# Performance work log

Measured on AMD Instinct MI355X. Metric: run time of the kernel, lower is better.

Reference implementation:

```python
import jax, jax.numpy as jnp
import numpy as np

N = 100_000      # nodes
E = 800_000      # edges (avg degree 8)
IN = 64          # in_channels
OUT = 64         # out_channels
HEADS = 4
HD = OUT // HEADS  # per-head out channels (concat=True)


def _unif(key, shape, fan_in):
    b = 1.0 / np.sqrt(fan_in)
    return jax.random.uniform(key, shape, jnp.float32, -b, b)


def setup_inputs() -> dict:
    key = jax.random.key(0)
    ks = jax.random.split(key, 12)
    x = jax.random.normal(ks[0], (N, IN), jnp.float32)
    pos = jax.random.normal(ks[1], (N, 3), jnp.float32)
    edge_index = jax.random.randint(ks[2], (2, E), 0, N, jnp.int32)
    # Per-head PointTransformerConv params (stacked over heads).
    # lin / lin_src / lin_dst are bias-free Linear(in, hd); pos_nn is Linear(3, hd) with bias.
    W_lin = _unif(ks[3], (HEADS, IN, HD), IN)
    W_src = _unif(ks[4], (HEADS, IN, HD), IN)
    W_dst = _unif(ks[5], (HEADS, IN, HD), IN)
    W_pos = _unif(ks[6], (HEADS, 3, HD), 3)
    b_pos = _unif(ks[7], (HEADS, HD), 3)
    # projection MLP: Linear(OUT,OUT) -> ReLU -> Linear(OUT,OUT)
    W1 = _unif(ks[8], (OUT, OUT), OUT)
    b1 = _unif(ks[9], (OUT,), OUT)
    W2 = _unif(ks[10], (OUT, OUT), OUT)
    b2 = _unif(ks[11], (OUT,), OUT)
    return dict(x=x, pos=pos, edge_index=edge_index, W_lin=W_lin, W_src=W_src,
                W_dst=W_dst, W_pos=W_pos, b_pos=b_pos, W1=W1, b1=b1, W2=W2, b2=b2)


def reference(x, pos, edge_index, W_lin, W_src, W_dst, W_pos, b_pos, W1, b1, W2, b2):
    # Add self-loops (PointTransformerConv default add_self_loops=True).
    loops = jnp.arange(N, dtype=edge_index.dtype)
    src = jnp.concatenate([edge_index[0], loops])   # j (source)
    dst = jnp.concatenate([edge_index[1], loops])   # i (target)

    # Per-node, all-heads projections: [N, H, HD]
    v = jnp.einsum('ni,hio->nho', x, W_lin)
    a_src = jnp.einsum('ni,hio->nho', x, W_src)
    a_dst = jnp.einsum('ni,hio->nho', x, W_dst)

    # Relative-position encoding delta = pos_nn(pos_i - pos_j): [Et, H, HD]
    rel = pos[dst] - pos[src]
    delta = jnp.einsum('ec,hco->eho', rel, W_pos) + b_pos

    # Attention logits per edge/channel: alpha_i - alpha_j + delta
    alpha = a_dst[dst] - a_src[src] + delta

    # Segment softmax over incoming edges of each target node (numerically stable).
    amax = jax.ops.segment_max(alpha, dst, num_segments=N)
    amax = jnp.where(jnp.isfinite(amax), amax, 0.0)
    ex = jnp.exp(alpha - amax[dst])
    denom = jax.ops.segment_sum(ex, dst, num_segments=N)
    attn = ex / jnp.maximum(denom[dst], 1e-16)

    # Message = attn * (lin(x_j) + delta), scatter-sum to targets: [N, H, HD]
    msg = attn * (v[src] + delta)
    out_h = jax.ops.segment_sum(msg, dst, num_segments=N)

    # Concat heads -> projection MLP
    out = out_h.reshape(N, HEADS * HD)
    h = jax.nn.relu(out @ W1 + b1)
    return h @ W2 + b2
```

## Files before the change

### kernel.cpp

```cpp
#include <hip/hip_runtime.h>
#include <math.h>


typedef _Float16 f16;
typedef _Float16 f16x2 __attribute__((ext_vector_type(2)));
typedef _Float16 f16x4 __attribute__((ext_vector_type(4)));
typedef _Float16 f16x8 __attribute__((ext_vector_type(8)));
typedef float f32x4 __attribute__((ext_vector_type(4)));

#define A_PITCH 104
#define C_PITCH 200
#define LOG2E 1.44269504f
#define S_CAP 32

__global__ __launch_bounds__(256) void zero_wprep_kernel(
    int Zb, int* __restrict__ cnt, int N,
    const float* __restrict__ Ws, const float* __restrict__ Wl,
    const float* __restrict__ Wp, const float* __restrict__ bp,
    const float* __restrict__ W1, const float* __restrict__ W2,
    f16* __restrict__ Bt, f16* __restrict__ W1p, f16* __restrict__ W2p)
{
    if ((int)blockIdx.x < Zb) {
        int i4 = (blockIdx.x * 256 + threadIdx.x) * 4;
        if (i4 + 3 < N) {
            *(int4*)&cnt[i4] = make_int4(0, 0, 0, 0);
        } else {
            for (int i = i4; i < N; i++) cnt[i] = 0;
        }
        return;
    }
    int idx = (blockIdx.x - Zb) * 256 + threadIdx.x;
    if (idx < 192 * 96) {
        int col = idx / 96, k = idx - col * 96;
        float v = 0.f;
        if (col < 128) {
            int p = col >> 1, h = p >> 4, o = p & 15;
            if (col & 1) {
                if (k < 64)      v = Wl[h * 1024 + k * 16 + o];
                else if (k < 67) v = -Wp[h * 48 + (k - 64) * 16 + o];
            } else {
                if (k < 64)      v = -LOG2E * Ws[h * 1024 + k * 16 + o];
                else if (k < 67) v = -LOG2E * Wp[h * 48 + (k - 64) * 16 + o];
            }
        } else {
            int c = col - 128, h = c >> 4, o = c & 15;
            if (k >= 64 && k < 67) v = Wp[h * 48 + (k - 64) * 16 + o];
            else if (k == 67)      v = bp[c];
        }
        Bt[col * 96 + k] = (f16)v;
    } else if (idx < 192 * 96 + 4096) {
        int t = idx - 192 * 96;
        int col = t >> 6, k = t & 63;
        W1p[col * 64 + k] = (f16)W1[k * 64 + col];
    } else if (idx < 192 * 96 + 8192) {
        int t = idx - 192 * 96 - 4096;
        int col = t >> 6, k = t & 63;
        W2p[col * 64 + k] = (f16)W2[k * 64 + col];
    }
}

__global__ __launch_bounds__(256) void gemm_hist_kernel(
    const float* __restrict__ x, const float* __restrict__ pos,
    const f16* __restrict__ Bt,
    f16* __restrict__ AV, f16* __restrict__ G, int N, int Gb,
    const int* __restrict__ ei, int E, int Hb2,
    int* __restrict__ cnt, int* __restrict__ ssrc)
{
    __shared__ f16 smem[64 * C_PITCH];
    int tid = threadIdx.x;

    if (blockIdx.x & 1) {
        int hb = blockIdx.x >> 1;
        if (hb >= Hb2) return;
        int e0 = hb * 512 + tid;
        int e1 = e0 + 256;
        int s0 = 0, d0 = 0, s1 = 0, d1 = 0;
        bool a0 = e0 < E, a1 = e1 < E;
        if (a0) { s0 = ei[e0]; d0 = ei[E + e0]; }
        if (a1) { s1 = ei[e1]; d1 = ei[E + e1]; }
        if (a0) {
            int r = atomicAdd(&cnt[d0], 1);
            if (r < S_CAP) ssrc[d0 * S_CAP + r] = s0;
        }
        if (a1) {
            int r = atomicAdd(&cnt[d1], 1);
            if (r < S_CAP) ssrc[d1 * S_CAP + r] = s1;
        }
        return;
    }

    int gb = blockIdx.x >> 1;
    if (gb >= Gb) return;
    int l = tid & 63, wv = tid >> 6;
    int quad = l >> 4, lr = l & 15;
    int nb = gb * 64;

    for (int it = 0; it < 4; it++) {
        int q = it * 256 + tid;
        int n = q >> 4, k = (q & 15) * 4;
        float4 xv = make_float4(0.f, 0.f, 0.f, 0.f);
        if (nb + n < N) xv = *(const float4*)&x[(size_t)(nb + n) * 64 + k];
        f16x4 h4; h4[0] = (f16)xv.x; h4[1] = (f16)xv.y; h4[2] = (f16)xv.z; h4[3] = (f16)xv.w;
        *(f16x4*)&smem[n * A_PITCH + k] = h4;
    }
    {
        int n = tid >> 2, seg = tid & 3;
        f16x4 z = {(f16)0, (f16)0, (f16)0, (f16)0};
        f16x4 h4 = z;
        if (seg == 0 && nb + n < N) {
            h4[0] = (f16)pos[(size_t)(nb + n) * 3 + 0];
            h4[1] = (f16)pos[(size_t)(nb + n) * 3 + 1];
            h4[2] = (f16)pos[(size_t)(nb + n) * 3 + 2];
            h4[3] = (f16)1.0f;
        }
        *(f16x4*)&smem[n * A_PITCH + 64 + seg * 8] = h4;
        *(f16x4*)&smem[n * A_PITCH + 64 + seg * 8 + 4] = z;
    }
    __syncthreads();

    f16x8 af[4][3];
    #pragma unroll
    for (int mt = 0; mt < 4; mt++)
        #pragma unroll
        for (int kt = 0; kt < 3; kt++)
            af[mt][kt] = *(const f16x8*)&smem[(mt * 16 + lr) * A_PITCH + kt * 32 + quad * 8];
    __syncthreads();

    #pragma unroll
    for (int t = 0; t < 3; t++) {
        int colBase = (wv * 3 + t) * 16;
        f16x8 b0 = *(const f16x8*)&Bt[(colBase + lr) * 96 + 0  + quad * 8];
        f16x8 b1 = *(const f16x8*)&Bt[(colBase + lr) * 96 + 32 + quad * 8];
        f16x8 b2 = *(const f16x8*)&Bt[(colBase + lr) * 96 + 64 + quad * 8];
        #pragma unroll
        for (int mt = 0; mt < 4; mt++) {
            f32x4 acc = {0.f, 0.f, 0.f, 0.f};
            acc = __builtin_amdgcn_mfma_f32_16x16x32_f16(af[mt][0], b0, acc, 0, 0, 0);
            acc = __builtin_amdgcn_mfma_f32_16x16x32_f16(af[mt][1], b1, acc, 0, 0, 0);
            acc = __builtin_amdgcn_mfma_f32_16x16x32_f16(af[mt][2], b2, acc, 0, 0, 0);
            int col = colBase + lr;
            #pragma unroll
            for (int r = 0; r < 4; r++) {
                int row = mt * 16 + quad * 4 + r;
                smem[row * C_PITCH + col] = (f16)acc[r];
            }
        }
    }
    __syncthreads();

    for (int it = 0; it < 4; it++) {
        int cid = it * 256 + tid;
        int row = cid >> 4, off = (cid & 15) * 8;
        if (nb + row < N)
            *(f16x8*)&AV[(size_t)(nb + row) * 128 + off] =
                *(const f16x8*)&smem[row * C_PITCH + off];
    }
    for (int it = 0; it < 2; it++) {
        int cid = it * 256 + tid;
        int row = cid >> 3, off = (cid & 7) * 8;
        if (nb + row < N)
            *(f16x8*)&G[(size_t)(nb + row) * 64 + off] =
                *(const f16x8*)&smem[row * C_PITCH + 128 + off];
    }
}

__global__ __launch_bounds__(256) void attn_mlp_kernel(
    const f16* __restrict__ AV, const f16* __restrict__ G,
    const int* __restrict__ cnt, const int* __restrict__ ssrc,
    const f16* __restrict__ W1p, const f16* __restrict__ W2p,
    const float* __restrict__ b1, const float* __restrict__ b2,
    float* __restrict__ out, int N)
{
    __shared__ f16 As[32 * 72];
    __shared__ f16 Hs[32 * 72];
    int tid = threadIdx.x, c = tid & 63, wv = tid >> 6;
    int quad = c >> 4, lr = c & 15;
    int nb = blockIdx.x * 32;

    const f16x2* AV2 = (const f16x2*)AV;

    for (int t = 0; t < 8; t++) {
        int i = __builtin_amdgcn_readfirstlane(nb + wv * 8 + t);
        float oh = 0.f;
        if (i < N) {
            float Gi = (float)G[(size_t)i * 64 + c];
            f16x2 wi = AV2[(size_t)i * 64 + c];
            float e0 = __builtin_amdgcn_exp2f((float)wi[0]);
            float num = e0 * (float)wi[1];
            float den = e0;
            int deg = __builtin_amdgcn_readfirstlane(cnt[i]);
            if (deg > S_CAP) deg = S_CAP;
            int base = i * S_CAP;
            for (int k = 0; k < deg; k += 8) {
                int j[8];
                #pragma unroll
                for (int s = 0; s < 8; s++) {
                    int jj = __builtin_amdgcn_readfirstlane(ssrc[base + k + s]);
                    jj = jj < 0 ? 0 : (jj >= N ? N - 1 : jj);
                    j[s] = jj;
                }
                f16x2 w[8];
                #pragma unroll
                for (int s = 0; s < 8; s++) w[s] = AV2[(size_t)j[s] * 64 + c];
                #pragma unroll
                for (int s = 0; s < 8; s++) {
                    float e = __builtin_amdgcn_exp2f((float)w[s][0]);
                    e = (k + s < deg) ? e : 0.f;
                    num = fmaf(e, (float)w[s][1], num);
                    den += e;
                }
            }
            oh = num / den + Gi;
        }
        As[(wv * 8 + t) * 72 + c] = (f16)oh;
    }
    __syncthreads();

    f16x8 af[2][2];
    #pragma unroll
    for (int mt = 0; mt < 2; mt++)
        #pragma unroll
        for (int kt = 0; kt < 2; kt++)
            af[mt][kt] = *(const f16x8*)&As[(mt * 16 + lr) * 72 + kt * 32 + quad * 8];

    int col = wv * 16 + lr;
    f16x8 wb0 = *(const f16x8*)&W1p[col * 64 + quad * 8];
    f16x8 wb1 = *(const f16x8*)&W1p[col * 64 + 32 + quad * 8];
    float bias1 = b1[col];
    #pragma unroll
    for (int mt = 0; mt < 2; mt++) {
        f32x4 acc = {0.f, 0.f, 0.f, 0.f};
        acc = __builtin_amdgcn_mfma_f32_16x16x32_f16(af[mt][0], wb0, acc, 0, 0, 0);
        acc = __builtin_amdgcn_mfma_f32_16x16x32_f16(af[mt][1], wb1, acc, 0, 0, 0);
        #pragma unroll
        for (int r = 0; r < 4; r++) {
            int row = mt * 16 + quad * 4 + r;
            Hs[row * 72 + col] = (f16)fmaxf(acc[r] + bias1, 0.f);
        }
    }
    __syncthreads();

    f16x8 ag[2][2];
    #pragma unroll
    for (int mt = 0; mt < 2; mt++)
        #pragma unroll
        for (int kt = 0; kt < 2; kt++)
            ag[mt][kt] = *(const f16x8*)&Hs[(mt * 16 + lr) * 72 + kt * 32 + quad * 8];

    f16x8 wc0 = *(const f16x8*)&W2p[col * 64 + quad * 8];
    f16x8 wc1 = *(const f16x8*)&W2p[col * 64 + 32 + quad * 8];
    float bias2 = b2[col];
    #pragma unroll
    for (int mt = 0; mt < 2; mt++) {
        f32x4 acc = {0.f, 0.f, 0.f, 0.f};
        acc = __builtin_amdgcn_mfma_f32_16x16x32_f16(ag[mt][0], wc0, acc, 0, 0, 0);
        acc = __builtin_amdgcn_mfma_f32_16x16x32_f16(ag[mt][1], wc1, acc, 0, 0, 0);
        #pragma unroll
        for (int r = 0; r < 4; r++) {
            int row = nb + mt * 16 + quad * 4 + r;
            if (row < N) out[(size_t)row * 64 + col] = acc[r] + bias2;
        }
    }
}

extern "C" void kernel_launch(void* const* d_in, const int* in_sizes, int n_in,
                              void* d_out, int out_size, void* d_ws, size_t ws_size,
                              hipStream_t stream)
{
    const float* x    = (const float*)d_in[0];
    const float* pos  = (const float*)d_in[1];
    const int*   ei   = (const int*)d_in[2];
    const float* Wl   = (const float*)d_in[3];
    const float* Ws   = (const float*)d_in[4];
    const float* Wp   = (const float*)d_in[6];
    const float* bpos = (const float*)d_in[7];
    const float* W1   = (const float*)d_in[8];
    const float* b1   = (const float*)d_in[9];
    const float* W2   = (const float*)d_in[10];
    const float* b2   = (const float*)d_in[11];
    float* out = (float*)d_out;

    const int N = in_sizes[0] / 64;
    const int E = in_sizes[2] / 2;

    char* w = (char*)d_ws;
    f16*  AV   = (f16*)w;                   w += (size_t)N * 128 * 2;
    f16*  G    = (f16*)w;                   w += (size_t)N * 64 * 2;
    f16*  Bt   = (f16*)w;                   w += 192 * 96 * 2;
    f16*  W1p  = (f16*)w;                   w += 4096 * 2;
    f16*  W2p  = (f16*)w;                   w += 4096 * 2;
    int*  cnt  = (int*)w;                   w += (size_t)N * 4;
    int*  ssrc = (int*)w;                   w += (size_t)N * S_CAP * 4;

    const int Zb  = (N + 1023) / 1024;
    const int Pb  = (192 * 96 + 8192 + 255) / 256;
    const int Gb  = (N + 63) / 64;
    const int Hb2 = (E + 511) / 512;
    const int Kb  = (Gb > Hb2 ? Gb : Hb2) * 2;

    zero_wprep_kernel<<<Zb + Pb, 256, 0, stream>>>(Zb, cnt, N, Ws, Wl, Wp, bpos,
                                                   W1, W2, Bt, W1p, W2p);
    gemm_hist_kernel<<<Kb, 256, 0, stream>>>(x, pos, Bt, AV, G, N, Gb,
                                             ei, E, Hb2, cnt, ssrc);
    attn_mlp_kernel<<<(N + 31) / 32, 256, 0, stream>>>(AV, G, cnt, ssrc, W1p, W2p,
                                                       b1, b2, out, N);
}
```

Baseline: 180.2 us.

## Precompute exp weights per source node and gather two targets at once

The projection kernel now applies exp2 to each source node's logit once and stores the pair (e, e*v) in AV, replacing the raw (logit, value) pair. The attention kernel then only sums the gathered pairs instead of running exp per edge. It also processes two target nodes per iteration, interleaving their gathers to keep more memory loads in flight. The cost is that exp values are stored in fp16 with no max subtraction, which risks overflow or precision loss. Out-of-range neighbour indices are also now mapped to 0 rather than clamped.

```diff
diff --git a/kernel.cpp b/kernel.cpp
--- a/kernel.cpp
+++ b/kernel.cpp
@@ -151,9 +151,18 @@
     for (int it = 0; it < 4; it++) {
         int cid = it * 256 + tid;
         int row = cid >> 4, off = (cid & 15) * 8;
-        if (nb + row < N)
-            *(f16x8*)&AV[(size_t)(nb + row) * 128 + off] =
-                *(const f16x8*)&smem[row * C_PITCH + off];
+        if (nb + row < N) {
+            f16x8 w8 = *(const f16x8*)&smem[row * C_PITCH + off];
+            f16x8 o;
+            #pragma unroll
+            for (int p = 0; p < 4; p++) {
+                float e  = __builtin_amdgcn_exp2f((float)w8[2 * p]);
+                float ev = e * (float)w8[2 * p + 1];
+                o[2 * p]     = (f16)e;
+                o[2 * p + 1] = (f16)ev;
+            }
+            *(f16x8*)&AV[(size_t)(nb + row) * 128 + off] = o;
+        }
     }
     for (int it = 0; it < 2; it++) {
         int cid = it * 256 + tid;
@@ -179,40 +188,60 @@
 
     const f16x2* AV2 = (const f16x2*)AV;
 
-    for (int t = 0; t < 8; t++) {
-        int i = __builtin_amdgcn_readfirstlane(nb + wv * 8 + t);
-        float oh = 0.f;
-        if (i < N) {
-            float Gi = (float)G[(size_t)i * 64 + c];
-            f16x2 wi = AV2[(size_t)i * 64 + c];
-            float e0 = __builtin_amdgcn_exp2f((float)wi[0]);
-            float num = e0 * (float)wi[1];
-            float den = e0;
-            int deg = __builtin_amdgcn_readfirstlane(cnt[i]);
-            if (deg > S_CAP) deg = S_CAP;
-            int base = i * S_CAP;
-            for (int k = 0; k < deg; k += 8) {
-                int j[8];
+    for (int pt = 0; pt < 4; pt++) {
+        int i0 = __builtin_amdgcn_readfirstlane(nb + wv * 8 + pt * 2);
+        int i1 = i0 + 1;
+        if (i1 >= N) i1 = N - 1;
+        if (i0 >= N) i0 = N - 1;
+        int deg0 = __builtin_amdgcn_readfirstlane(cnt[i0]); if (deg0 > S_CAP) deg0 = S_CAP;
+        int deg1 = __builtin_amdgcn_readfirstlane(cnt[i1]); if (deg1 > S_CAP) deg1 = S_CAP;
+        float Gi0 = (float)G[(size_t)i0 * 64 + c];
+        float Gi1 = (float)G[(size_t)i1 * 64 + c];
+        f16x2 sv0 = AV2[(size_t)i0 * 64 + c];
+        f16x2 sv1 = AV2[(size_t)i1 * 64 + c];
+        float den0 = (float)sv0[0], num0 = (float)sv0[1];
+        float den1 = (float)sv1[0], num1 = (float)sv1[1];
+        int base0 = i0 * S_CAP, base1 = i1 * S_CAP;
+
+        for (int b = 0; b < S_CAP; b += 8) {
+            bool r0 = b < deg0, r1 = b < deg1;
+            if (!(r0 | r1)) break;
+            f16x2 w0[8], w1[8];
+            if (r0) {
                 #pragma unroll
                 for (int s = 0; s < 8; s++) {
-                    int jj = __builtin_amdgcn_readfirstlane(ssrc[base + k + s]);
-                    jj = jj < 0 ? 0 : (jj >= N ? N - 1 : jj);
-                    j[s] = jj;
+                    int jj = __builtin_amdgcn_readfirstlane(ssrc[base0 + b + s]);
+                    if ((unsigned)jj >= (unsigned)N) jj = 0;
+                    w0[s] = AV2[(size_t)jj * 64 + c];
                 }
-                f16x2 w[8];
-                #pragma unroll
-                for (int s = 0; s < 8; s++) w[s] = AV2[(size_t)j[s] * 64 + c];
+            }
+            if (r1) {
                 #pragma unroll
                 for (int s = 0; s < 8; s++) {
-                    float e = __builtin_amdgcn_exp2f((float)w[s][0]);
-                    e = (k + s < deg) ? e : 0.f;
-                    num = fmaf(e, (float)w[s][1], num);
-                    den += e;
+                    int jj = __builtin_amdgcn_readfirstlane(ssrc[base1 + b + s]);
+                    if ((unsigned)jj >= (unsigned)N) jj = 0;
+                    w1[s] = AV2[(size_t)jj * 64 + c];
                 }
             }
-            oh = num / den + Gi;
-        }
-        As[(wv * 8 + t) * 72 + c] = (f16)oh;
+            if (r0) {
+                #pragma unroll
+                for (int s = 0; s < 8; s++) {
+                    bool ok = (b + s) < deg0;
+                    den0 += ok ? (float)w0[s][0] : 0.f;
+                    num0 += ok ? (float)w0[s][1] : 0.f;
+                }
+            }
+            if (r1) {
+                #pragma unroll
+                for (int s = 0; s < 8; s++) {
+                    bool ok = (b + s) < deg1;
+                    den1 += ok ? (float)w1[s][0] : 0.f;
+                    num1 += ok ? (float)w1[s][1] : 0.f;
+                }
+            }
+        }
+        As[(wv * 8 + pt * 2) * 72 + c]     = (f16)(num0 / den0 + Gi0);
+        As[(wv * 8 + pt * 2 + 1) * 72 + c] = (f16)(num1 / den1 + Gi1);
     }
     __syncthreads();
 
```

Result: no change. 178.9 us (-0.7%).
